# Kernel tuning notes

Hardware: AMD Instinct MI355X
Metric: run time of the kernel (lower is better)

## Reference

```python
import jax, jax.numpy as jnp
import numpy as np

RARITY_ALPHA = 0.5


def _forward(obs_emb, observed_mask, lengths, avg_interval, var_prior_emb_tensor,
             rarity_W, adjI, p2s_W1, p2s_b1, p2s_W2, p2s_b2,
             Wu, bu, Wr, br, Wc, bc):
    B, T, N, D = obs_emb.shape
    I = jnp.eye(N, dtype=obs_emb.dtype)
    # hypernetwork conditioning vector per node (prior_to_state MLP); identical
    # across batch since var_prior_emb_tensor is repeated over the batch dim.
    vv = jax.nn.relu(var_prior_emb_tensor @ p2s_W1 + p2s_b1) @ p2s_W2 + p2s_b2  # [N,E]
    vv = jnp.broadcast_to(vv[None], (B, N, vv.shape[-1]))                        # [B,N,E]
    tot = observed_mask.sum(axis=1)  # var_total_obs [B,N]

    def gate(z, W, b):
        # MLP_Param: per-node weights W_n = sum_e vv[n,e]*W[e]; fused einsum avoids
        # materializing [B,N,2D+1,D].
        return jnp.einsum('bni,bne,eio->bno', z, vv, W) + jnp.einsum('bne,eo->bno', vv, b)

    def step_fn(carry, xs):
        h, out = carry
        cur_obs, m, cur_avg, step = xs  # [B,N,D], [B,N], [B,N], scalar
        rs = RARITY_ALPHA * jnp.tanh(cur_avg / (tot + 1.0))                  # [B,N]
        rmat = -rarity_W * jnp.abs(rs[:, :, None] - rs[:, None, :])          # [B,N,N]
        # adj_mask[b,i,j] = observed(b,i)*observed(b,j)  (column-set then row-zero)
        adj_mask = m[:, :, None] * m[:, None, :]
        cur_adj = adjI * (1.0 + rmat) * adj_mask * (1.0 - I) + I             # [B,N,N]
        x = jnp.concatenate([cur_obs, rs[..., None]], axis=-1)              # [B,N,D+1]
        comb = jnp.einsum('bij,bjf->bif', cur_adj,
                          jnp.concatenate([x, h], axis=-1))                  # [B,N,2D+1]
        r = jax.nn.sigmoid(gate(comb, Wr, br))
        u = jax.nn.sigmoid(gate(comb, Wu, bu))
        mm = m[..., None] > 0
        h1 = jnp.where(mm, r * h, h)                      # h[nodes_ind] = r*h[nodes_ind]
        cand = jnp.tanh(gate(jnp.concatenate([x, h1], axis=-1), Wc, bc))
        h2 = jnp.where(mm, (1.0 - u) * h1 + u * cand, h1)  # scatter back at observed nodes
        out = jnp.where((step == lengths - 1)[:, None, None], h2, out)
        return (h2, out), None

    h0 = jnp.zeros((B, N, D), obs_emb.dtype)
    xs = (obs_emb.transpose(1, 0, 2, 3), observed_mask.transpose(1, 0, 2),
          avg_interval.transpose(1, 0, 2), jnp.arange(T))
    (_, out), _ = jax.lax.scan(step_fn, (h0, jnp.zeros_like(h0)), xs)
    return out


def setup_inputs() -> dict:
    B, T, N, D, E = 32, 64, 128, 64, 5
    key = jax.random.key(0)
    ks = jax.random.split(key, 18)
    inp = {}
    inp['obs_emb'] = jax.random.normal(ks[0], (B, T, N, D), jnp.float32)
    inp['adj'] = jax.random.normal(ks[1], (N, N), jnp.float32)  # unused by forward
    inp['observed_mask'] = (jax.random.uniform(ks[2], (B, T, N)) < 0.5).astype(jnp.float32)
    inp['observed_tp'] = jax.random.uniform(ks[3], (B, T), jnp.float32)       # unused
    inp['tp_emb_tensor'] = jax.random.normal(ks[4], (B, T, 1), jnp.float32)   # unused
    inp['lengths'] = jax.random.randint(ks[5], (B,), T // 2, T + 1, jnp.int32)
    inp['avg_interval'] = jax.random.uniform(ks[6], (B, T, N), jnp.float32)
    inp['var_prior_emb_tensor'] = jax.random.normal(ks[7], (N, 768), jnp.float32)
    # learned parameters
    inp['rarity_W'] = jax.random.normal(ks[8], (N, N), jnp.float32)
    inp['adjI'] = jnp.eye(N, dtype=jnp.float32) + 0.01 * jax.random.normal(ks[9], (N, N), jnp.float32)
    inp['p2s_W1'] = 0.05 * jax.random.normal(ks[10], (768, 2 * D), jnp.float32)
    inp['p2s_b1'] = jnp.zeros((2 * D,), jnp.float32)
    inp['p2s_W2'] = 0.1 * jax.random.normal(ks[11], (2 * D, E), jnp.float32)
    inp['p2s_b2'] = jnp.zeros((E,), jnp.float32)
    inp['Wu'] = 0.1 * jax.random.normal(ks[12], (E, 2 * D + 1, D), jnp.float32)
    inp['bu'] = 0.1 * jax.random.normal(ks[13], (E, D), jnp.float32)
    inp['Wr'] = 0.1 * jax.random.normal(ks[14], (E, 2 * D + 1, D), jnp.float32)
    inp['br'] = 0.1 * jax.random.normal(ks[15], (E, D), jnp.float32)
    inp['Wc'] = 0.1 * jax.random.normal(ks[16], (E, 2 * D + 1, D), jnp.float32)
    inp['bc'] = 0.1 * jax.random.normal(ks[17], (E, D), jnp.float32)
    return inp


def reference(obs_emb, adj, observed_mask, observed_tp, tp_emb_tensor, lengths,
              avg_interval, var_prior_emb_tensor, rarity_W, adjI, p2s_W1, p2s_b1,
              p2s_W2, p2s_b2, Wu, bu, Wr, br, Wc, bc):
    # adj, observed_tp, tp_emb_tensor are accepted but never used, as in the torch code
    return _forward(obs_emb, observed_mask, lengths, avg_interval, var_prior_emb_tensor,
                    rarity_W, adjI, p2s_W1, p2s_b1, p2s_W2, p2s_b2,
                    Wu, bu, Wr, br, Wc, bc)
```

## Files before the change

### kernel.cpp

```cpp
#include <hip/hip_runtime.h>
#include <math.h>

constexpr size_t WS_VV  = 1024;
constexpr size_t WS_TOT = 2048;
constexpr size_t WS_RS  = 8192;
constexpr size_t WS_WH  = 270336;
constexpr size_t WS_WX  = 1843200;
constexpr size_t WS_BF  = 3440640;
constexpr size_t WS_H   = 3465216;
constexpr size_t CXSZ   = 2129920;
constexpr size_t GXSZ   = 2097152;
constexpr size_t WS_CX0 = 3727360;
constexpr size_t WS_GXR0= 7987200;
constexpr size_t WS_GXU0= 12181504;
constexpr size_t WS_CXC0= 16375808;

__device__ __forceinline__ float sigm(float x){ return 1.f/(1.f+expf(-x)); }

__device__ __forceinline__ float2 ld2_mall(const float* p){
  union { unsigned long long u; float2 f; } cv;
  cv.u = __hip_atomic_load((const unsigned long long*)p, __ATOMIC_RELAXED,
                           __HIP_MEMORY_SCOPE_AGENT);
  return cv.f;
}
__device__ __forceinline__ void st2_mall(float* p, float a, float b){
  union { unsigned long long u; float2 f; } cv;
  cv.f = make_float2(a, b);
  __hip_atomic_store((unsigned long long*)p, cv.u, __ATOMIC_RELAXED,
                     __HIP_MEMORY_SCOPE_AGENT);
}

__global__ void k_vv(const float* __restrict__ vpe, const float* __restrict__ W1,
                     const float* __restrict__ b1, const float* __restrict__ W2,
                     const float* __restrict__ b2, float* __restrict__ ws){
  int n = blockIdx.x, tid = threadIdx.x;
  __shared__ float hid[128];
  if (tid < 128){
    float acc = b1[tid];
    for (int k=0;k<768;k++) acc = fmaf(vpe[n*768+k], W1[k*128+tid], acc);
    hid[tid] = fmaxf(acc, 0.f);
  }
  __syncthreads();
  if (tid < 5){
    float acc = b2[tid];
    for (int h=0;h<128;h++) acc = fmaf(hid[h], W2[h*5+tid], acc);
    ws[WS_VV + n*5 + tid] = acc;
  }
}

__global__ void k_fold(const float* __restrict__ Wr, const float* __restrict__ Wu,
                       const float* __restrict__ Wc, const float* __restrict__ br,
                       const float* __restrict__ bu, const float* __restrict__ bc,
                       float* __restrict__ ws){
  int bid = blockIdx.x; int g = bid>>7; int n = bid&127;
  const float* W  = (g==0)?Wr:(g==1)?Wu:Wc;
  const float* bb = (g==0)?br:(g==1)?bu:bc;
  float v[5];
#pragma unroll
  for (int e=0;e<5;e++) v[e] = ws[WS_VV + n*5 + e];
  for (int idx=threadIdx.x; idx<129*64; idx+=256){
    int i = idx>>6, o = idx&63;
    float a = 0.f;
#pragma unroll
    for (int e=0;e<5;e++) a = fmaf(v[e], W[(e*129+i)*64+o], a);
    if (i < 65) ws[WS_WX + (size_t)(g*128+n)*4160 + i*64 + o] = a;
    else        ws[WS_WH + (size_t)(g*128+n)*4096 + (i-65)*64 + o] = a;
  }
  if (threadIdx.x < 64){
    int o = threadIdx.x; float a = 0.f;
#pragma unroll
    for (int e=0;e<5;e++) a = fmaf(v[e], bb[e*64+o], a);
    ws[WS_BF + (g*128+n)*64 + o] = a;
  }
}

__global__ void k_tot(const float* __restrict__ mask, float* __restrict__ ws){
  int id = blockIdx.x*256 + threadIdx.x;
  int b = id>>7, n = id&127;
  float s = 0.f;
  for (int t=0;t<64;t++) s += mask[(b*64+t)*128 + n];
  ws[WS_TOT + b*128 + n] = s;
}

__global__ void k_rs(const float* __restrict__ avg, float* __restrict__ ws){
  int id = blockIdx.x*256 + threadIdx.x;
  int b = id>>13, n = id&127;
  float tot = ws[WS_TOT + b*128 + n];
  ws[WS_RS + id] = 0.5f * tanhf(avg[id] / (tot + 1.f));
}

__device__ void p4a_body(float* smem, const float* __restrict__ obs,
      const float* __restrict__ mask, const float* __restrict__ adjI,
      const float* __restrict__ rW, const int* __restrict__ lengths,
      float* __restrict__ ws, int cc, int rc){
  int b = rc>>3, tl = rc&7, t = cc*8 + tl;
  if (t >= lengths[b]) return;
  int rt = b*64 + t;
  float* xt   = smem;
  float* adjh = smem + 4352;
  float* rs_l = smem + 13056;
  float* m_l  = smem + 13184;
  int tid = threadIdx.x;
  if (tid < 128){ rs_l[tid] = ws[WS_RS + rt*128 + tid]; m_l[tid] = mask[rt*128 + tid]; }
  __syncthreads();
  int it = tid>>3, ft = tid&7, i0 = it*4, f0 = ft*8;
  float4 aL[4], aH[4]; float a64[4];
#pragma unroll
  for (int ii=0;ii<4;ii++){ aL[ii]=make_float4(0,0,0,0); aH[ii]=make_float4(0,0,0,0); a64[ii]=0.f; }
  for (int half=0; half<2; half++){
    __syncthreads();
    int j0 = half*64;
    for (int idx=tid; idx<4096; idx+=256){
      int jl = idx>>6, f = idx&63;
      xt[jl*68+f] = obs[(size_t)rt*8192 + (j0+jl)*64 + f];
    }
    if (tid < 64) xt[tid*68+64] = rs_l[j0+tid];
    for (int idx=tid; idx<8192; idx+=256){
      int i = idx>>6, jl = idx&63, j = j0+jl;
      float a;
      if (i == j) a = 1.f;
      else {
        int gi = i*128 + j;
        float dd = fabsf(rs_l[i] - rs_l[j]);
        a = adjI[gi] * (1.f - rW[gi]*dd) * m_l[i] * m_l[j];
      }
      adjh[i*68+jl] = a;
    }
    __syncthreads();
    for (int jb=0; jb<16; jb++){
      float4 av[4];
#pragma unroll
      for (int ii=0;ii<4;ii++) av[ii] = *(const float4*)&adjh[(i0+ii)*68 + jb*4];
#pragma unroll
      for (int jj=0;jj<4;jj++){
        int jl = jb*4 + jj;
        float4 xlo = *(const float4*)&xt[jl*68 + f0];
        float4 xhi = *(const float4*)&xt[jl*68 + f0 + 4];
        float xr = xt[jl*68 + 64];
#pragma unroll
        for (int ii=0;ii<4;ii++){
          float a = (jj==0)?av[ii].x:(jj==1)?av[ii].y:(jj==2)?av[ii].z:av[ii].w;
          aL[ii].x = fmaf(a, xlo.x, aL[ii].x); aL[ii].y = fmaf(a, xlo.y, aL[ii].y);
          aL[ii].z = fmaf(a, xlo.z, aL[ii].z); aL[ii].w = fmaf(a, xlo.w, aL[ii].w);
          aH[ii].x = fmaf(a, xhi.x, aH[ii].x); aH[ii].y = fmaf(a, xhi.y, aH[ii].y);
          aH[ii].z = fmaf(a, xhi.z, aH[ii].z); aH[ii].w = fmaf(a, xhi.w, aH[ii].w);
          a64[ii] = fmaf(a, xr, a64[ii]);
        }
      }
    }
  }
  size_t cxb = WS_CX0 + (size_t)(cc&1)*CXSZ;
#pragma unroll
  for (int ii=0;ii<4;ii++){
    int i = i0 + ii;
    size_t base = cxb + (size_t)i*16640 + (size_t)rc*65 + f0;
    ws[base+0]=aL[ii].x; ws[base+1]=aL[ii].y; ws[base+2]=aL[ii].z; ws[base+3]=aL[ii].w;
    ws[base+4]=aH[ii].x; ws[base+5]=aH[ii].y; ws[base+6]=aH[ii].z; ws[base+7]=aH[ii].w;
    if (ft == 0) ws[cxb + (size_t)i*16640 + (size_t)rc*65 + 64] = a64[ii];
  }
}

__device__ void p4b_body(float* smem, const float* __restrict__ obs,
      const int* __restrict__ lengths, float* __restrict__ ws, int cc, int pbid){
  int g = pbid >> 8; int r2 = pbid & 255; int n = r2 >> 1; int tile = r2 & 1;
  float* A  = smem;
  float* Wl = smem + 8832;
  float* bl = smem + 12992;
  int* slen = (int*)(smem + 13056);
  int tid = threadIdx.x;
  if (tid < 32) slen[tid] = lengths[tid];
  for (int idx=tid; idx<4160; idx+=256) Wl[idx] = ws[WS_WX + (size_t)(g*128+n)*4160 + idx];
  if (tid < 64) bl[tid] = ws[WS_BF + (g*128+n)*64 + tid];
  size_t cxb = WS_CX0 + (size_t)(cc&1)*CXSZ;
  if (g < 2){
    const float* src = &ws[cxb + (size_t)n*16640 + (size_t)tile*8320];
    for (int idx=tid; idx<8320; idx+=256){
      int r = idx/65, f = idx - r*65;
      A[r*69+f] = src[idx];
    }
  } else {
    for (int idx=tid; idx<8320; idx+=256){
      int r = idx/65, f = idx - r*65;
      int grow = tile*128 + r;
      int gb = grow>>3, t = cc*8 + (grow&7);
      float v = (f < 64) ? obs[(size_t)(gb*64+t)*8192 + n*64 + f]
                         : ws[WS_RS + (gb*64+t)*128 + n];
      A[r*69+f] = v;
    }
  }
  __syncthreads();
  int rt8 = tid>>4, dq = tid&15;
  float4 acc[8];
#pragma unroll
  for (int rr=0;rr<8;rr++) acc[rr] = make_float4(0,0,0,0);
  for (int k=0;k<65;k++){
    float4 w = *(const float4*)&Wl[k*64 + dq*4];
#pragma unroll
    for (int rr=0;rr<8;rr++){
      float a = A[(rt8*8+rr)*69 + k];
      acc[rr].x = fmaf(a,w.x,acc[rr].x); acc[rr].y = fmaf(a,w.y,acc[rr].y);
      acc[rr].z = fmaf(a,w.z,acc[rr].z); acc[rr].w = fmaf(a,w.w,acc[rr].w);
    }
  }
  float4 b4 = *(const float4*)&bl[dq*4];
  size_t gxb = ((g==0)?WS_GXR0:(g==1)?WS_GXU0:WS_CXC0) + (size_t)(cc&1)*GXSZ;
#pragma unroll
  for (int rr=0;rr<8;rr++){
    int grow = tile*128 + rt8*8 + rr;
    int gb = grow>>3, gtl = grow&7;
    if (cc*8 + gtl < slen[gb]){
      float4 o; o.x=acc[rr].x+b4.x; o.y=acc[rr].y+b4.y; o.z=acc[rr].z+b4.z; o.w=acc[rr].w+b4.w;
      *(float4*)&ws[gxb + ((size_t)(n*8+gtl)*32 + gb)*64 + dq*4] = o;
    }
  }
}

__device__ void krec_body(float* smem, const float* __restrict__ mask,
      const int* __restrict__ lengths, const float* __restrict__ adjI,
      const float* __restrict__ rWm, float* __restrict__ out,
      float* __restrict__ ws, int c){
  __builtin_amdgcn_s_setprio(1);
  unsigned* hfl = (unsigned*)ws;
  const int bid = blockIdx.x, tid = threadIdx.x;
  const int bA = bid>>3, s = bid&7, ns = s*16;
  float* hs   = smem;
  float* adjT = smem + 8192;
  float* chT  = smem + 10752;
  float* hT   = smem + 11840;
  float* rs_l = smem + 12928;
  float* m_l  = smem + 13056;
  const int lenA = lengths[bA];
  const int ng = tid>>6, fA = tid&63;
  const int nl = tid>>4, fq = tid&15;
  const int n  = ns + nl;
  float* hbuf = &ws[WS_H];
  const float* wrg = &ws[WS_WH + (size_t)(0*128+n)*4096];
  const float* wug = &ws[WS_WH + (size_t)(1*128+n)*4096];
  const float* wcg = &ws[WS_WH + (size_t)(2*128+n)*4096];
  const int c0 = c*8;
  const size_t gq = (size_t)(c&1)*GXSZ;

  for (int t=c0; t<c0+8; t++){
    if (t >= lenA){
      if (tid == 0)
        __hip_atomic_store(&hfl[bid], (unsigned)(t+1), __ATOMIC_RELAXED,
                           __HIP_MEMORY_SCOPE_AGENT);
      __syncthreads();
      continue;
    }
    if (tid < 128) rs_l[tid] = ws[WS_RS + (size_t)(bA*64+t)*128 + tid];
    else           m_l[tid-128] = mask[(size_t)(bA*64+t)*128 + (tid-128)];
    __syncthreads();
    for (int idx=tid; idx<2048; idx+=256){
      int j = idx&127, il = idx>>7, I = ns+il;
      float a;
      if (I == j) a = 1.f;
      else {
        int gi = I*128 + j;
        float dd = fabsf(rs_l[I] - rs_l[j]);
        a = adjI[gi]*(1.f - rWm[gi]*dd)*m_l[I]*m_l[j];
      }
      adjT[j*20 + il] = a;
    }
    const int tl = t - c0;
    size_t gof = ((size_t)(n*8+tl)*32 + bA)*64 + fq*4;
    float4 arv = *(const float4*)&ws[WS_GXR0 + gq + gof];
    float4 auv = *(const float4*)&ws[WS_GXU0 + gq + gof];
    float4 acv = *(const float4*)&ws[WS_CXC0 + gq + gof];
    float  msv = m_l[n];
    if (t > 0){
      if (tid < 8){
        unsigned tgt = (unsigned)t; int guard = 0;
        while (__hip_atomic_load(&hfl[bA*8 + tid], __ATOMIC_RELAXED,
                 __HIP_MEMORY_SCOPE_AGENT) < tgt && ++guard < (1<<20))
          __builtin_amdgcn_s_sleep(2);
      }
    }
    __syncthreads();
#pragma unroll
    for (int k=0;k<16;k++){
      int p = tid + 256*k;
      float2 v = ld2_mall(&hbuf[(size_t)bA*8192 + 2*p]);
      *(float2*)&hs[2*p] = v;
    }
    __syncthreads();
    float acc[4] = {0.f,0.f,0.f,0.f};
#pragma unroll 4
    for (int j=0;j<128;j++){
      float hv = hs[j*64 + fA];
      float4 a4 = *(const float4*)&adjT[j*20 + ng*4];
      acc[0] = fmaf(a4.x, hv, acc[0]);
      acc[1] = fmaf(a4.y, hv, acc[1]);
      acc[2] = fmaf(a4.z, hv, acc[2]);
      acc[3] = fmaf(a4.w, hv, acc[3]);
    }
#pragma unroll
    for (int r=0;r<4;r++) chT[(ng*4+r)*68 + fA] = acc[r];
    __syncthreads();
#pragma unroll 4
    for (int k=0;k<64;k++){
      float cv = chT[nl*68 + k];
      float4 wr4 = *(const float4*)&wrg[k*64 + fq*4];
      float4 wu4 = *(const float4*)&wug[k*64 + fq*4];
      arv.x = fmaf(cv,wr4.x,arv.x); arv.y = fmaf(cv,wr4.y,arv.y);
      arv.z = fmaf(cv,wr4.z,arv.z); arv.w = fmaf(cv,wr4.w,arv.w);
      auv.x = fmaf(cv,wu4.x,auv.x); auv.y = fmaf(cv,wu4.y,auv.y);
      auv.z = fmaf(cv,wu4.z,auv.z); auv.w = fmaf(cv,wu4.w,auv.w);
    }
    float4 rr4, uu4, h1;
    rr4.x = sigm(arv.x); rr4.y = sigm(arv.y); rr4.z = sigm(arv.z); rr4.w = sigm(arv.w);
    uu4.x = sigm(auv.x); uu4.y = sigm(auv.y); uu4.z = sigm(auv.z); uu4.w = sigm(auv.w);
    float4 hown = *(const float4*)&hs[n*64 + fq*4];
    bool ob = msv > 0.f;
    h1.x = ob ? rr4.x*hown.x : hown.x;
    h1.y = ob ? rr4.y*hown.y : hown.y;
    h1.z = ob ? rr4.z*hown.z : hown.z;
    h1.w = ob ? rr4.w*hown.w : hown.w;
    *(float4*)&hT[nl*68 + fq*4] = h1;
    __syncthreads();
#pragma unroll 4
    for (int k=0;k<64;k++){
      float hv1 = hT[nl*68 + k];
      float4 wc4 = *(const float4*)&wcg[k*64 + fq*4];
      acv.x = fmaf(hv1,wc4.x,acv.x); acv.y = fmaf(hv1,wc4.y,acv.y);
      acv.z = fmaf(hv1,wc4.z,acv.z); acv.w = fmaf(hv1,wc4.w,acv.w);
    }
    float4 cd, h2;
    cd.x = tanhf(acv.x); cd.y = tanhf(acv.y); cd.z = tanhf(acv.z); cd.w = tanhf(acv.w);
    h2.x = ob ? (1.f-uu4.x)*h1.x + uu4.x*cd.x : h1.x;
    h2.y = ob ? (1.f-uu4.y)*h1.y + uu4.y*cd.y : h1.y;
    h2.z = ob ? (1.f-uu4.z)*h1.z + uu4.z*cd.z : h1.z;
    h2.w = ob ? (1.f-uu4.w)*h1.w + uu4.w*cd.w : h1.w;
    float* hp = &hbuf[((size_t)bA*128 + n)*64 + fq*4];
    st2_mall(hp,   h2.x, h2.y);
    st2_mall(hp+2, h2.z, h2.w);
    if (t == lenA-1)
      *(float4*)&out[((size_t)bA*128 + n)*64 + fq*4] = h2;
    __syncthreads();
    asm volatile("s_waitcnt vmcnt(0)" ::: "memory");
    if (tid == 0)
      __hip_atomic_store(&hfl[bid], (unsigned)(t+1), __ATOMIC_RELAXED,
                         __HIP_MEMORY_SCOPE_AGENT);
  }
}

__global__ __launch_bounds__(256) void p4a_k(const float* __restrict__ obs,
      const float* __restrict__ mask, const float* __restrict__ adjI,
      const float* __restrict__ rW, const int* __restrict__ lengths,
      float* __restrict__ ws, int cc){
  __shared__ float smem[13312];
  p4a_body(smem, obs, mask, adjI, rW, lengths, ws, cc, blockIdx.x);
}
__global__ __launch_bounds__(256) void p4b_k(const float* __restrict__ obs,
      const int* __restrict__ lengths, float* __restrict__ ws, int cc){
  __shared__ float smem[13312];
  p4b_body(smem, obs, lengths, ws, cc, blockIdx.x);
}

__global__ __launch_bounds__(256) void kfused(const float* __restrict__ obs,
      const float* __restrict__ mask, const float* __restrict__ adjI,
      const float* __restrict__ rW, const int* __restrict__ lengths,
      float* __restrict__ out, float* __restrict__ ws, int c){
  __shared__ float smem[13312];
  int bid = blockIdx.x;
  if (bid < 256){
    krec_body(smem, mask, lengths, adjI, rW, out, ws, c);
    return;
  }
  bool has4a = (c < 6);
  if (has4a && bid < 512){
    p4a_body(smem, obs, mask, adjI, rW, lengths, ws, c+2, bid-256);
    return;
  }
  int pb = bid - (has4a ? 512 : 256);
  p4b_body(smem, obs, lengths, ws, c+1, pb);
}

extern "C" void kernel_launch(void* const* d_in, const int* in_sizes, int n_in,
                              void* d_out, int out_size, void* d_ws, size_t ws_size,
                              hipStream_t stream){
  const float* obs  = (const float*)d_in[0];
  const float* maskp= (const float*)d_in[2];
  const int*   lens = (const int*)d_in[5];
  const float* avg  = (const float*)d_in[6];
  const float* vpe  = (const float*)d_in[7];
  const float* rW   = (const float*)d_in[8];
  const float* adjI = (const float*)d_in[9];
  const float* W1   = (const float*)d_in[10];
  const float* b1   = (const float*)d_in[11];
  const float* W2   = (const float*)d_in[12];
  const float* b2   = (const float*)d_in[13];
  const float* Wu   = (const float*)d_in[14];
  const float* bu   = (const float*)d_in[15];
  const float* Wr   = (const float*)d_in[16];
  const float* br   = (const float*)d_in[17];
  const float* Wc   = (const float*)d_in[18];
  const float* bc   = (const float*)d_in[19];
  float* out = (float*)d_out;
  float* ws  = (float*)d_ws;
  hipMemsetAsync(d_ws, 0, 4096, stream);
  hipMemsetAsync((char*)d_ws + WS_H*sizeof(float), 0, 262144*sizeof(float), stream);
  k_vv  <<<128, 256, 0, stream>>>(vpe, W1, b1, W2, b2, ws);
  k_fold<<<384, 256, 0, stream>>>(Wr, Wu, Wc, br, bu, bc, ws);
  k_tot <<<16,  256, 0, stream>>>(maskp, ws);
  k_rs  <<<1024,256, 0, stream>>>(avg, ws);
  p4a_k<<<256, 256, 0, stream>>>(obs, maskp, adjI, rW, lens, ws, 0);
  p4a_k<<<256, 256, 0, stream>>>(obs, maskp, adjI, rW, lens, ws, 1);
  p4b_k<<<768, 256, 0, stream>>>(obs, lens, ws, 0);
  for (int c = 0; c < 8; c++){
    int grid = (c <= 5) ? 1280 : (c == 6) ? 1024 : 256;
    kfused<<<grid, 256, 0, stream>>>(obs, maskp, adjI, rW, lens, out, ws, c);
  }
}
```

Baseline: 1.432 ms.

## Assign recurrent-step work roles dynamically by XCD so batch siblings share a die

Each recurrence block now reads its XCD id from a hardware register and claims a (batch, node-slice) role through an atomic counter and a compare-and-swap claim table. The table is laid out so that the eight slices of one batch tend to land on the same XCD. The goal is to keep the per-step hidden-state exchange and flag polling between sibling blocks inside one L2 instead of crossing dies. The cost is extra atomics at block start and reliance on claim and counter state in the workspace being set up correctly for each chunk c. Flags are now indexed by role rather than by block id.

```diff
diff --git a/kernel.cpp b/kernel.cpp
--- a/kernel.cpp
+++ b/kernel.cpp
@@ -221,14 +221,39 @@
       float* __restrict__ ws, int c){
   __builtin_amdgcn_s_setprio(1);
   unsigned* hfl = (unsigned*)ws;
-  const int bid = blockIdx.x, tid = threadIdx.x;
-  const int bA = bid>>3, s = bid&7, ns = s*16;
+  const int tid = threadIdx.x;
   float* hs   = smem;
   float* adjT = smem + 8192;
   float* chT  = smem + 10752;
   float* hT   = smem + 11840;
   float* rs_l = smem + 12928;
   float* m_l  = smem + 13056;
+  int* role_sh = (int*)(smem + 13184);
+
+  if (tid == 0){
+    unsigned xcd = __builtin_amdgcn_s_getreg(14356) & 7;
+    unsigned* claim = (unsigned*)ws + 256;
+    unsigned* ctr   = (unsigned*)ws + 520 + c*8;
+    unsigned r = __hip_atomic_fetch_add(&ctr[xcd], 1u, __ATOMIC_RELAXED,
+                                        __HIP_MEMORY_SCOPE_AGENT);
+    int start = (int)(xcd*32u + (r & 31u));
+    int got = -1;
+    for (int i=0; i<256; i++){
+      int slot = (start + i) & 255;
+      unsigned exp = (unsigned)c;
+      if (__hip_atomic_compare_exchange_strong(&claim[slot], &exp, (unsigned)(c+1),
+            __ATOMIC_RELAXED, __ATOMIC_RELAXED, __HIP_MEMORY_SCOPE_AGENT)){
+        got = slot; break;
+      }
+    }
+    if (got < 0) got = (int)(blockIdx.x & 255);
+    *role_sh = got;
+  }
+  __syncthreads();
+  const int role = *role_sh;
+  const int bA = role & 31, s = role >> 5, ns = s*16;
+  const int fidx = bA*8 + s;
+
   const int lenA = lengths[bA];
   const int ng = tid>>6, fA = tid&63;
   const int nl = tid>>4, fq = tid&15;
@@ -243,7 +268,7 @@
   for (int t=c0; t<c0+8; t++){
     if (t >= lenA){
       if (tid == 0)
-        __hip_atomic_store(&hfl[bid], (unsigned)(t+1), __ATOMIC_RELAXED,
+        __hip_atomic_store(&hfl[fidx], (unsigned)(t+1), __ATOMIC_RELAXED,
                            __HIP_MEMORY_SCOPE_AGENT);
       __syncthreads();
       continue;
@@ -339,7 +364,7 @@
     __syncthreads();
     asm volatile("s_waitcnt vmcnt(0)" ::: "memory");
     if (tid == 0)
-      __hip_atomic_store(&hfl[bid], (unsigned)(t+1), __ATOMIC_RELAXED,
+      __hip_atomic_store(&hfl[fidx], (unsigned)(t+1), __ATOMIC_RELAXED,
                          __HIP_MEMORY_SCOPE_AGENT);
   }
 }
```

After: 1.430 ms. No clear change (-0.2%).

## Split recurrent work so each block handles two batches with eight nodes each

Applied to the files above, without the earlier changes.

Each recurrent block now covers eight nodes for a pair of batch elements instead of sixteen nodes for one batch element. Per-batch flags are indexed by sixteen slices, and the next batch's hidden state is prefetched into registers while the first batch's graph aggregation runs. Each block syncs with sixteen producer slices per batch rather than eight, which adds cross-block dependencies. The per-node weight reads are now shared across two batches.

```diff
diff --git a/kernel.cpp b/kernel.cpp
--- a/kernel.cpp
+++ b/kernel.cpp
@@ -222,17 +222,20 @@
   __builtin_amdgcn_s_setprio(1);
   unsigned* hfl = (unsigned*)ws;
   const int bid = blockIdx.x, tid = threadIdx.x;
-  const int bA = bid>>3, s = bid&7, ns = s*16;
+  const int bp = bid>>4, sl = bid&15, ns = sl*8;
+  const int b0 = 2*bp, b1 = 2*bp+1;
   float* hs   = smem;
   float* adjT = smem + 8192;
-  float* chT  = smem + 10752;
-  float* hT   = smem + 11840;
-  float* rs_l = smem + 12928;
-  float* m_l  = smem + 13056;
-  const int lenA = lengths[bA];
+  float* chT  = smem + 10240;
+  float* hT   = smem + 11328;
+  float* rs_l = smem + 12416;
+  float* m_l  = smem + 12672;
+  const int len0 = lengths[b0], len1 = lengths[b1];
   const int ng = tid>>6, fA = tid&63;
-  const int nl = tid>>4, fq = tid&15;
+  const int bl = tid>>7, nl = (tid>>4)&7, fq = tid&15;
   const int n  = ns + nl;
+  const int bg = 2*bp + bl;
+  const int mylen = bl ? len1 : len0;
   float* hbuf = &ws[WS_H];
   const float* wrg = &ws[WS_WH + (size_t)(0*128+n)*4096];
   const float* wug = &ws[WS_WH + (size_t)(1*128+n)*4096];
@@ -241,105 +244,154 @@
   const size_t gq = (size_t)(c&1)*GXSZ;
 
   for (int t=c0; t<c0+8; t++){
-    if (t >= lenA){
-      if (tid == 0)
-        __hip_atomic_store(&hfl[bid], (unsigned)(t+1), __ATOMIC_RELAXED,
+    const bool alive0 = (t < len0), alive1 = (t < len1);
+    if (!alive0 && !alive1){
+      if (tid < 2)
+        __hip_atomic_store(&hfl[(b0+tid)*16 + sl], (unsigned)(t+1), __ATOMIC_RELAXED,
                            __HIP_MEMORY_SCOPE_AGENT);
       __syncthreads();
       continue;
     }
-    if (tid < 128) rs_l[tid] = ws[WS_RS + (size_t)(bA*64+t)*128 + tid];
-    else           m_l[tid-128] = mask[(size_t)(bA*64+t)*128 + (tid-128)];
+    {
+      int bb = tid>>7, j = tid&127;
+      bool al = bb ? alive1 : alive0;
+      int bt = (2*bp+bb)*64 + t;
+      rs_l[tid] = al ? ws[WS_RS + (size_t)bt*128 + j] : 0.f;
+      m_l[tid]  = al ? mask[(size_t)bt*128 + j] : 0.f;
+    }
     __syncthreads();
     for (int idx=tid; idx<2048; idx+=256){
-      int j = idx&127, il = idx>>7, I = ns+il;
+      int bb = idx>>10, j = (idx>>3)&127, il = idx&7, I = ns+il;
       float a;
       if (I == j) a = 1.f;
       else {
         int gi = I*128 + j;
-        float dd = fabsf(rs_l[I] - rs_l[j]);
-        a = adjI[gi]*(1.f - rWm[gi]*dd)*m_l[I]*m_l[j];
-      }
-      adjT[j*20 + il] = a;
+        float dd = fabsf(rs_l[bb*128+I] - rs_l[bb*128+j]);
+        a = adjI[gi]*(1.f - rWm[gi]*dd)*m_l[bb*128+I]*m_l[bb*128+j];
+      }
+      adjT[(bb*128+j)*8 + il] = a;
     }
     const int tl = t - c0;
-    size_t gof = ((size_t)(n*8+tl)*32 + bA)*64 + fq*4;
-    float4 arv = *(const float4*)&ws[WS_GXR0 + gq + gof];
-    float4 auv = *(const float4*)&ws[WS_GXU0 + gq + gof];
-    float4 acv = *(const float4*)&ws[WS_CXC0 + gq + gof];
-    float  msv = m_l[n];
-    if (t > 0){
-      if (tid < 8){
+    const bool myalive = (t < mylen);
+    size_t gof = ((size_t)(n*8+tl)*32 + bg)*64 + fq*4;
+    float4 arv = make_float4(0,0,0,0), auv = arv, acv = arv;
+    if (myalive){
+      arv = *(const float4*)&ws[WS_GXR0 + gq + gof];
+      auv = *(const float4*)&ws[WS_GXU0 + gq + gof];
+      acv = *(const float4*)&ws[WS_CXC0 + gq + gof];
+    }
+    const float msv = m_l[bl*128 + n];
+    if (t > 0 && tid < 32){
+      bool pal = (tid < 16) ? alive0 : alive1;
+      int pb  = (tid < 16) ? b0 : b1;
+      if (pal){
         unsigned tgt = (unsigned)t; int guard = 0;
-        while (__hip_atomic_load(&hfl[bA*8 + tid], __ATOMIC_RELAXED,
+        while (__hip_atomic_load(&hfl[pb*16 + (tid&15)], __ATOMIC_RELAXED,
                  __HIP_MEMORY_SCOPE_AGENT) < tgt && ++guard < (1<<20))
           __builtin_amdgcn_s_sleep(2);
       }
     }
     __syncthreads();
-#pragma unroll
-    for (int k=0;k<16;k++){
-      int p = tid + 256*k;
-      float2 v = ld2_mall(&hbuf[(size_t)bA*8192 + 2*p]);
-      *(float2*)&hs[2*p] = v;
-    }
-    __syncthreads();
-    float acc[4] = {0.f,0.f,0.f,0.f};
+    if (alive0){
+#pragma unroll
+      for (int k=0;k<16;k++){
+        int p = tid + 256*k;
+        *(float2*)&hs[2*p] = ld2_mall(&hbuf[(size_t)b0*8192 + 2*p]);
+      }
+    }
+    __syncthreads();
+    float4 hown = make_float4(0,0,0,0);
+    if (bl == 0 && alive0) hown = *(const float4*)&hs[n*64 + fq*4];
+    float2 pre[16];
+    if (alive1){
+#pragma unroll
+      for (int k=0;k<16;k++){
+        int p = tid + 256*k;
+        pre[k] = ld2_mall(&hbuf[(size_t)b1*8192 + 2*p]);
+      }
+    }
+    if (alive0){
+      float ac0 = 0.f, ac1 = 0.f;
 #pragma unroll 4
-    for (int j=0;j<128;j++){
-      float hv = hs[j*64 + fA];
-      float4 a4 = *(const float4*)&adjT[j*20 + ng*4];
-      acc[0] = fmaf(a4.x, hv, acc[0]);
-      acc[1] = fmaf(a4.y, hv, acc[1]);
-      acc[2] = fmaf(a4.z, hv, acc[2]);
-      acc[3] = fmaf(a4.w, hv, acc[3]);
-    }
-#pragma unroll
-    for (int r=0;r<4;r++) chT[(ng*4+r)*68 + fA] = acc[r];
-    __syncthreads();
+      for (int j=0;j<128;j++){
+        float hv = hs[j*64 + fA];
+        float2 a2 = *(const float2*)&adjT[j*8 + ng*2];
+        ac0 = fmaf(a2.x, hv, ac0);
+        ac1 = fmaf(a2.y, hv, ac1);
+      }
+      chT[(ng*2+0)*68 + fA] = ac0;
+      chT[(ng*2+1)*68 + fA] = ac1;
+    }
+    __syncthreads();
+    if (alive1){
+#pragma unroll
+      for (int k=0;k<16;k++){
+        int p = tid + 256*k;
+        *(float2*)&hs[2*p] = pre[k];
+      }
+    }
+    __syncthreads();
+    if (bl == 1 && alive1) hown = *(const float4*)&hs[n*64 + fq*4];
+    if (alive1){
+      float ac0 = 0.f, ac1 = 0.f;
 #pragma unroll 4
-    for (int k=0;k<64;k++){
-      float cv = chT[nl*68 + k];
-      float4 wr4 = *(const float4*)&wrg[k*64 + fq*4];
-      float4 wu4 = *(const float4*)&wug[k*64 + fq*4];
-      arv.x = fmaf(cv,wr4.x,arv.x); arv.y = fmaf(cv,wr4.y,arv.y);
-      arv.z = fmaf(cv,wr4.z,arv.z); arv.w = fmaf(cv,wr4.w,arv.w);
-      auv.x = fmaf(cv,wu4.x,auv.x); auv.y = fmaf(cv,wu4.y,auv.y);
-      auv.z = fmaf(cv,wu4.z,auv.z); auv.w = fmaf(cv,wu4.w,auv.w);
-    }
-    float4 rr4, uu4, h1;
-    rr4.x = sigm(arv.x); rr4.y = sigm(arv.y); rr4.z = sigm(arv.z); rr4.w = sigm(arv.w);
-    uu4.x = sigm(auv.x); uu4.y = sigm(auv.y); uu4.z = sigm(auv.z); uu4.w = sigm(auv.w);
-    float4 hown = *(const float4*)&hs[n*64 + fq*4];
-    bool ob = msv > 0.f;
-    h1.x = ob ? rr4.x*hown.x : hown.x;
-    h1.y = ob ? rr4.y*hown.y : hown.y;
-    h1.z = ob ? rr4.z*hown.z : hown.z;
-    h1.w = ob ? rr4.w*hown.w : hown.w;
-    *(float4*)&hT[nl*68 + fq*4] = h1;
-    __syncthreads();
+      for (int j=0;j<128;j++){
+        float hv = hs[j*64 + fA];
+        float2 a2 = *(const float2*)&adjT[(128+j)*8 + ng*2];
+        ac0 = fmaf(a2.x, hv, ac0);
+        ac1 = fmaf(a2.y, hv, ac1);
+      }
+      chT[(8 + ng*2+0)*68 + fA] = ac0;
+      chT[(8 + ng*2+1)*68 + fA] = ac1;
+    }
+    __syncthreads();
+    float4 rr4, uu4, h1 = hown;
+    if (myalive){
 #pragma unroll 4
-    for (int k=0;k<64;k++){
-      float hv1 = hT[nl*68 + k];
-      float4 wc4 = *(const float4*)&wcg[k*64 + fq*4];
-      acv.x = fmaf(hv1,wc4.x,acv.x); acv.y = fmaf(hv1,wc4.y,acv.y);
-      acv.z = fmaf(hv1,wc4.z,acv.z); acv.w = fmaf(hv1,wc4.w,acv.w);
-    }
-    float4 cd, h2;
-    cd.x = tanhf(acv.x); cd.y = tanhf(acv.y); cd.z = tanhf(acv.z); cd.w = tanhf(acv.w);
-    h2.x = ob ? (1.f-uu4.x)*h1.x + uu4.x*cd.x : h1.x;
-    h2.y = ob ? (1.f-uu4.y)*h1.y + uu4.y*cd.y : h1.y;
-    h2.z = ob ? (1.f-uu4.z)*h1.z + uu4.z*cd.z : h1.z;
-    h2.w = ob ? (1.f-uu4.w)*h1.w + uu4.w*cd.w : h1.w;
-    float* hp = &hbuf[((size_t)bA*128 + n)*64 + fq*4];
-    st2_mall(hp,   h2.x, h2.y);
-    st2_mall(hp+2, h2.z, h2.w);
-    if (t == lenA-1)
-      *(float4*)&out[((size_t)bA*128 + n)*64 + fq*4] = h2;
+      for (int k=0;k<64;k++){
+        float cv = chT[(bl*8+nl)*68 + k];
+        float4 wr4 = *(const float4*)&wrg[k*64 + fq*4];
+        float4 wu4 = *(const float4*)&wug[k*64 + fq*4];
+        arv.x = fmaf(cv,wr4.x,arv.x); arv.y = fmaf(cv,wr4.y,arv.y);
+        arv.z = fmaf(cv,wr4.z,arv.z); arv.w = fmaf(cv,wr4.w,arv.w);
+        auv.x = fmaf(cv,wu4.x,auv.x); auv.y = fmaf(cv,wu4.y,auv.y);
+        auv.z = fmaf(cv,wu4.z,auv.z); auv.w = fmaf(cv,wu4.w,auv.w);
+      }
+      rr4.x = sigm(arv.x); rr4.y = sigm(arv.y); rr4.z = sigm(arv.z); rr4.w = sigm(arv.w);
+      uu4.x = sigm(auv.x); uu4.y = sigm(auv.y); uu4.z = sigm(auv.z); uu4.w = sigm(auv.w);
+      bool ob = msv > 0.f;
+      h1.x = ob ? rr4.x*hown.x : hown.x;
+      h1.y = ob ? rr4.y*hown.y : hown.y;
+      h1.z = ob ? rr4.z*hown.z : hown.z;
+      h1.w = ob ? rr4.w*hown.w : hown.w;
+      *(float4*)&hT[(bl*8+nl)*68 + fq*4] = h1;
+    }
+    __syncthreads();
+    if (myalive){
+#pragma unroll 4
+      for (int k=0;k<64;k++){
+        float hv1 = hT[(bl*8+nl)*68 + k];
+        float4 wc4 = *(const float4*)&wcg[k*64 + fq*4];
+        acv.x = fmaf(hv1,wc4.x,acv.x); acv.y = fmaf(hv1,wc4.y,acv.y);
+        acv.z = fmaf(hv1,wc4.z,acv.z); acv.w = fmaf(hv1,wc4.w,acv.w);
+      }
+      float4 cd, h2;
+      cd.x = tanhf(acv.x); cd.y = tanhf(acv.y); cd.z = tanhf(acv.z); cd.w = tanhf(acv.w);
+      bool ob = msv > 0.f;
+      h2.x = ob ? (1.f-uu4.x)*h1.x + uu4.x*cd.x : h1.x;
+      h2.y = ob ? (1.f-uu4.y)*h1.y + uu4.y*cd.y : h1.y;
+      h2.z = ob ? (1.f-uu4.z)*h1.z + uu4.z*cd.z : h1.z;
+      h2.w = ob ? (1.f-uu4.w)*h1.w + uu4.w*cd.w : h1.w;
+      float* hp = &hbuf[((size_t)bg*128 + n)*64 + fq*4];
+      st2_mall(hp,   h2.x, h2.y);
+      st2_mall(hp+2, h2.z, h2.w);
+      if (t == mylen-1)
+        *(float4*)&out[((size_t)bg*128 + n)*64 + fq*4] = h2;
+    }
     __syncthreads();
     asm volatile("s_waitcnt vmcnt(0)" ::: "memory");
-    if (tid == 0)
-      __hip_atomic_store(&hfl[bid], (unsigned)(t+1), __ATOMIC_RELAXED,
+    if (tid < 2)
+      __hip_atomic_store(&hfl[(b0+tid)*16 + sl], (unsigned)(t+1), __ATOMIC_RELAXED,
                          __HIP_MEMORY_SCOPE_AGENT);
   }
 }
```

Result: slower. 1.651 ms (+15.3%).

## Split recurrent step across 16 blocks per batch with 8 nodes each

Applied to the files above, without the earlier changes.

The recurrent krec part now uses 16 blocks per batch element, each owning 8 nodes, instead of 8 blocks of 16 nodes. The flag array, the adjacency tile layout and the grid sizes are adjusted to match. Each block waits on 16 peer flags, and only half its threads do the gate matvecs. The aim is to spread the latency-critical sequential step over more CUs and shorten per-step work. The cost is more inter-block synchronization traffic, the full h broadcast being reloaded by twice as many blocks, and idle threads.

```diff
diff --git a/kernel.cpp b/kernel.cpp
--- a/kernel.cpp
+++ b/kernel.cpp
@@ -162,6 +162,7 @@
 
 __device__ void p4b_body(float* smem, const float* __restrict__ obs,
       const int* __restrict__ lengths, float* __restrict__ ws, int cc, int pbid){
+  if (pbid >= 768) return;
   int g = pbid >> 8; int r2 = pbid & 255; int n = r2 >> 1; int tile = r2 & 1;
   float* A  = smem;
   float* Wl = smem + 8832;
@@ -222,16 +223,17 @@
   __builtin_amdgcn_s_setprio(1);
   unsigned* hfl = (unsigned*)ws;
   const int bid = blockIdx.x, tid = threadIdx.x;
-  const int bA = bid>>3, s = bid&7, ns = s*16;
+  const int bA = bid>>4, sl = bid&15, ns = sl*8;
   float* hs   = smem;
   float* adjT = smem + 8192;
-  float* chT  = smem + 10752;
-  float* hT   = smem + 11840;
-  float* rs_l = smem + 12928;
-  float* m_l  = smem + 13056;
+  float* chT  = smem + 9216;
+  float* hT   = smem + 9760;
+  float* rs_l = smem + 10304;
+  float* m_l  = smem + 10432;
   const int lenA = lengths[bA];
   const int ng = tid>>6, fA = tid&63;
-  const int nl = tid>>4, fq = tid&15;
+  const int nl = (tid>>4)&7, fq = tid&15;
+  const bool gthr = tid < 128;
   const int n  = ns + nl;
   float* hbuf = &ws[WS_H];
   const float* wrg = &ws[WS_WH + (size_t)(0*128+n)*4096];
@@ -243,7 +245,7 @@
   for (int t=c0; t<c0+8; t++){
     if (t >= lenA){
       if (tid == 0)
-        __hip_atomic_store(&hfl[bid], (unsigned)(t+1), __ATOMIC_RELAXED,
+        __hip_atomic_store(&hfl[bA*16+sl], (unsigned)(t+1), __ATOMIC_RELAXED,
                            __HIP_MEMORY_SCOPE_AGENT);
       __syncthreads();
       continue;
@@ -251,7 +253,7 @@
     if (tid < 128) rs_l[tid] = ws[WS_RS + (size_t)(bA*64+t)*128 + tid];
     else           m_l[tid-128] = mask[(size_t)(bA*64+t)*128 + (tid-128)];
     __syncthreads();
-    for (int idx=tid; idx<2048; idx+=256){
+    for (int idx=tid; idx<1024; idx+=256){
       int j = idx&127, il = idx>>7, I = ns+il;
       float a;
       if (I == j) a = 1.f;
@@ -260,18 +262,21 @@
         float dd = fabsf(rs_l[I] - rs_l[j]);
         a = adjI[gi]*(1.f - rWm[gi]*dd)*m_l[I]*m_l[j];
       }
-      adjT[j*20 + il] = a;
+      adjT[j*8 + il] = a;
     }
     const int tl = t - c0;
     size_t gof = ((size_t)(n*8+tl)*32 + bA)*64 + fq*4;
-    float4 arv = *(const float4*)&ws[WS_GXR0 + gq + gof];
-    float4 auv = *(const float4*)&ws[WS_GXU0 + gq + gof];
-    float4 acv = *(const float4*)&ws[WS_CXC0 + gq + gof];
-    float  msv = m_l[n];
+    float4 arv = make_float4(0,0,0,0), auv = arv, acv = arv;
+    if (gthr){
+      arv = *(const float4*)&ws[WS_GXR0 + gq + gof];
+      auv = *(const float4*)&ws[WS_GXU0 + gq + gof];
+      acv = *(const float4*)&ws[WS_CXC0 + gq + gof];
+    }
+    const float msv = m_l[n];
     if (t > 0){
-      if (tid < 8){
+      if (tid < 16){
         unsigned tgt = (unsigned)t; int guard = 0;
-        while (__hip_atomic_load(&hfl[bA*8 + tid], __ATOMIC_RELAXED,
+        while (__hip_atomic_load(&hfl[bA*16 + tid], __ATOMIC_RELAXED,
                  __HIP_MEMORY_SCOPE_AGENT) < tgt && ++guard < (1<<20))
           __builtin_amdgcn_s_sleep(2);
       }
@@ -280,66 +285,70 @@
 #pragma unroll
     for (int k=0;k<16;k++){
       int p = tid + 256*k;
-      float2 v = ld2_mall(&hbuf[(size_t)bA*8192 + 2*p]);
-      *(float2*)&hs[2*p] = v;
-    }
-    __syncthreads();
-    float acc[4] = {0.f,0.f,0.f,0.f};
+      *(float2*)&hs[2*p] = ld2_mall(&hbuf[(size_t)bA*8192 + 2*p]);
+    }
+    __syncthreads();
+    {
+      float ac0 = 0.f, ac1 = 0.f;
 #pragma unroll 4
-    for (int j=0;j<128;j++){
-      float hv = hs[j*64 + fA];
-      float4 a4 = *(const float4*)&adjT[j*20 + ng*4];
-      acc[0] = fmaf(a4.x, hv, acc[0]);
-      acc[1] = fmaf(a4.y, hv, acc[1]);
-      acc[2] = fmaf(a4.z, hv, acc[2]);
-      acc[3] = fmaf(a4.w, hv, acc[3]);
-    }
-#pragma unroll
-    for (int r=0;r<4;r++) chT[(ng*4+r)*68 + fA] = acc[r];
-    __syncthreads();
+      for (int j=0;j<128;j++){
+        float hv = hs[j*64 + fA];
+        float2 a2 = *(const float2*)&adjT[j*8 + ng*2];
+        ac0 = fmaf(a2.x, hv, ac0);
+        ac1 = fmaf(a2.y, hv, ac1);
+      }
+      chT[(ng*2+0)*68 + fA] = ac0;
+      chT[(ng*2+1)*68 + fA] = ac1;
+    }
+    __syncthreads();
+    float4 rr4, uu4, h1 = make_float4(0,0,0,0);
+    if (gthr){
 #pragma unroll 4
-    for (int k=0;k<64;k++){
-      float cv = chT[nl*68 + k];
-      float4 wr4 = *(const float4*)&wrg[k*64 + fq*4];
-      float4 wu4 = *(const float4*)&wug[k*64 + fq*4];
-      arv.x = fmaf(cv,wr4.x,arv.x); arv.y = fmaf(cv,wr4.y,arv.y);
-      arv.z = fmaf(cv,wr4.z,arv.z); arv.w = fmaf(cv,wr4.w,arv.w);
-      auv.x = fmaf(cv,wu4.x,auv.x); auv.y = fmaf(cv,wu4.y,auv.y);
-      auv.z = fmaf(cv,wu4.z,auv.z); auv.w = fmaf(cv,wu4.w,auv.w);
-    }
-    float4 rr4, uu4, h1;
-    rr4.x = sigm(arv.x); rr4.y = sigm(arv.y); rr4.z = sigm(arv.z); rr4.w = sigm(arv.w);
-    uu4.x = sigm(auv.x); uu4.y = sigm(auv.y); uu4.z = sigm(auv.z); uu4.w = sigm(auv.w);
-    float4 hown = *(const float4*)&hs[n*64 + fq*4];
-    bool ob = msv > 0.f;
-    h1.x = ob ? rr4.x*hown.x : hown.x;
-    h1.y = ob ? rr4.y*hown.y : hown.y;
-    h1.z = ob ? rr4.z*hown.z : hown.z;
-    h1.w = ob ? rr4.w*hown.w : hown.w;
-    *(float4*)&hT[nl*68 + fq*4] = h1;
-    __syncthreads();
+      for (int k=0;k<64;k++){
+        float cv = chT[nl*68 + k];
+        float4 wr4 = *(const float4*)&wrg[k*64 + fq*4];
+        float4 wu4 = *(const float4*)&wug[k*64 + fq*4];
+        arv.x = fmaf(cv,wr4.x,arv.x); arv.y = fmaf(cv,wr4.y,arv.y);
+        arv.z = fmaf(cv,wr4.z,arv.z); arv.w = fmaf(cv,wr4.w,arv.w);
+        auv.x = fmaf(cv,wu4.x,auv.x); auv.y = fmaf(cv,wu4.y,auv.y);
+        auv.z = fmaf(cv,wu4.z,auv.z); auv.w = fmaf(cv,wu4.w,auv.w);
+      }
+      rr4.x = sigm(arv.x); rr4.y = sigm(arv.y); rr4.z = sigm(arv.z); rr4.w = sigm(arv.w);
+      uu4.x = sigm(auv.x); uu4.y = sigm(auv.y); uu4.z = sigm(auv.z); uu4.w = sigm(auv.w);
+      float4 hown = *(const float4*)&hs[n*64 + fq*4];
+      bool ob = msv > 0.f;
+      h1.x = ob ? rr4.x*hown.x : hown.x;
+      h1.y = ob ? rr4.y*hown.y : hown.y;
+      h1.z = ob ? rr4.z*hown.z : hown.z;
+      h1.w = ob ? rr4.w*hown.w : hown.w;
+      *(float4*)&hT[nl*68 + fq*4] = h1;
+    }
+    __syncthreads();
+    if (gthr){
 #pragma unroll 4
-    for (int k=0;k<64;k++){
-      float hv1 = hT[nl*68 + k];
-      float4 wc4 = *(const float4*)&wcg[k*64 + fq*4];
-      acv.x = fmaf(hv1,wc4.x,acv.x); acv.y = fmaf(hv1,wc4.y,acv.y);
-      acv.z = fmaf(hv1,wc4.z,acv.z); acv.w = fmaf(hv1,wc4.w,acv.w);
-    }
-    float4 cd, h2;
-    cd.x = tanhf(acv.x); cd.y = tanhf(acv.y); cd.z = tanhf(acv.z); cd.w = tanhf(acv.w);
-    h2.x = ob ? (1.f-uu4.x)*h1.x + uu4.x*cd.x : h1.x;
-    h2.y = ob ? (1.f-uu4.y)*h1.y + uu4.y*cd.y : h1.y;
-    h2.z = ob ? (1.f-uu4.z)*h1.z + uu4.z*cd.z : h1.z;
-    h2.w = ob ? (1.f-uu4.w)*h1.w + uu4.w*cd.w : h1.w;
-    float* hp = &hbuf[((size_t)bA*128 + n)*64 + fq*4];
-    st2_mall(hp,   h2.x, h2.y);
-    st2_mall(hp+2, h2.z, h2.w);
-    if (t == lenA-1)
-      *(float4*)&out[((size_t)bA*128 + n)*64 + fq*4] = h2;
+      for (int k=0;k<64;k++){
+        float hv1 = hT[nl*68 + k];
+        float4 wc4 = *(const float4*)&wcg[k*64 + fq*4];
+        acv.x = fmaf(hv1,wc4.x,acv.x); acv.y = fmaf(hv1,wc4.y,acv.y);
+        acv.z = fmaf(hv1,wc4.z,acv.z); acv.w = fmaf(hv1,wc4.w,acv.w);
+      }
+      float4 cd, h2;
+      cd.x = tanhf(acv.x); cd.y = tanhf(acv.y); cd.z = tanhf(acv.z); cd.w = tanhf(acv.w);
+      bool ob = msv > 0.f;
+      h2.x = ob ? (1.f-uu4.x)*h1.x + uu4.x*cd.x : h1.x;
+      h2.y = ob ? (1.f-uu4.y)*h1.y + uu4.y*cd.y : h1.y;
+      h2.z = ob ? (1.f-uu4.z)*h1.z + uu4.z*cd.z : h1.z;
+      h2.w = ob ? (1.f-uu4.w)*h1.w + uu4.w*cd.w : h1.w;
+      float* hp = &hbuf[((size_t)bA*128 + n)*64 + fq*4];
+      st2_mall(hp,   h2.x, h2.y);
+      st2_mall(hp+2, h2.z, h2.w);
+      if (t == lenA-1)
+        *(float4*)&out[((size_t)bA*128 + n)*64 + fq*4] = h2;
+    }
     __syncthreads();
     asm volatile("s_waitcnt vmcnt(0)" ::: "memory");
     if (tid == 0)
-      __hip_atomic_store(&hfl[bid], (unsigned)(t+1), __ATOMIC_RELAXED,
+      __hip_atomic_store(&hfl[bA*16+sl], (unsigned)(t+1), __ATOMIC_RELAXED,
                          __HIP_MEMORY_SCOPE_AGENT);
   }
 }
@@ -363,16 +372,16 @@
       float* __restrict__ out, float* __restrict__ ws, int c){
   __shared__ float smem[13312];
   int bid = blockIdx.x;
-  if (bid < 256){
+  if (bid < 512){
     krec_body(smem, mask, lengths, adjI, rW, out, ws, c);
     return;
   }
   bool has4a = (c < 6);
-  if (has4a && bid < 512){
-    p4a_body(smem, obs, mask, adjI, rW, lengths, ws, c+2, bid-256);
+  if (has4a && bid < 768){
+    p4a_body(smem, obs, mask, adjI, rW, lengths, ws, c+2, bid-512);
     return;
   }
-  int pb = bid - (has4a ? 512 : 256);
+  int pb = bid - (has4a ? 768 : 512);
   p4b_body(smem, obs, lengths, ws, c+1, pb);
 }
 
@@ -408,7 +417,7 @@
   p4a_k<<<256, 256, 0, stream>>>(obs, maskp, adjI, rW, lens, ws, 1);
   p4b_k<<<768, 256, 0, stream>>>(obs, lens, ws, 0);
   for (int c = 0; c < 8; c++){
-    int grid = (c <= 5) ? 1280 : (c == 6) ? 1024 : 256;
+    int grid = (c <= 5) ? 1536 : (c == 6) ? 1280 : 512;
     kfused<<<grid, 256, 0, stream>>>(obs, maskp, adjI, rW, lens, out, ws, c);
   }
 }
```

Measured after the change: 1.462 ms. 2.1% more time.
